# Kernel tuning notes

Hardware: AMD Instinct MI355X
Metric: run time of the kernel (lower is better)

## Reference

```python
import jax, jax.numpy as jnp
import numpy as np

NA, NT, E = 8000, 30000, 150000
H, C, HID = 4, 64, 64  # heads, per-head out_channels, hidden_dim
AF, TF = 32, 48


def _gat(x_src, x_dst, src, dst, W, a_src, a_dst, bias, n_dst):
    # PyG GATConv, concat=False, add_self_loops=False, eval (no dropout)
    h_src = (x_src @ W).reshape(-1, H, C)          # [Ns,H,C]
    h_dst = (x_dst @ W).reshape(-1, H, C)          # [Nd,H,C]
    al_s = jnp.sum(h_src * a_src, axis=-1)         # [Ns,H]
    al_d = jnp.sum(h_dst * a_dst, axis=-1)         # [Nd,H]
    e = jax.nn.leaky_relu(al_s[src] + al_d[dst], 0.2)  # [E,H]
    m = jax.ops.segment_max(e, dst, num_segments=n_dst)
    m = jnp.where(jnp.isfinite(m), m, 0.0)
    ex = jnp.exp(e - m[dst])
    den = jax.ops.segment_sum(ex, dst, num_segments=n_dst)
    alpha = ex / (den[dst] + 1e-16)                # per-dst softmax
    out = jax.ops.segment_sum(alpha[:, :, None] * h_src[src], dst, num_segments=n_dst)
    return jnp.mean(out, axis=1) + bias            # mean over heads + bias


def _bn(x, g, b):  # BatchNorm1d, training-mode batch stats, biased var
    mu = jnp.mean(x, axis=0)
    v = jnp.var(x, axis=0)
    return g * (x - mu) * jax.lax.rsqrt(v + 1e-5) + b


def _ln(x, g, b):
    mu = jnp.mean(x, axis=-1, keepdims=True)
    v = jnp.var(x, axis=-1, keepdims=True)
    return g * (x - mu) * jax.lax.rsqrt(v + 1e-5) + b


def setup_inputs() -> dict:
    key = jax.random.key(0)
    ks = jax.random.split(key, 40)
    n = lambda i, shp, s=0.05: jax.random.normal(ks[i], shp, jnp.float32) * s
    ri = lambda i, hi: jax.random.randint(ks[i], (E,), 0, hi, jnp.int32)
    inp = {
        'x_agent': jax.random.normal(ks[0], (NA, AF), jnp.float32),
        'x_track': jax.random.normal(ks[1], (NT, TF), jnp.float32),
        'ei_a2t1_src': ri(2, NA), 'ei_a2t1_dst': ri(3, NT),
        'ei_t2a1_src': ri(4, NT), 'ei_t2a1_dst': ri(5, NA),
        'ei_a2t2_src': ri(6, NA), 'ei_a2t2_dst': ri(7, NT),
        'ei_t2a2_src': ri(8, NT), 'ei_t2a2_dst': ri(9, NA),
        'ae_W': n(10, (AF, HID)), 'ae_b': jnp.zeros((HID,), jnp.float32),
        'te_W': n(11, (TF, HID)), 'te_b': jnp.zeros((HID,), jnp.float32),
        # stacked GATConv params: [layer=3, relation=4, ...]; rel order: a2t1,t2a1,a2t2,t2a2
        'conv_W': n(12, (3, 4, HID, H * C)),
        'conv_asrc': n(13, (3, 4, H, C)),
        'conv_adst': n(14, (3, 4, H, C)),
        'conv_bias': jnp.zeros((3, 4, C), jnp.float32),
        'bn_gamma': jnp.ones((3, 2, HID), jnp.float32),   # [layer, agent/track, HID]
        'bn_beta': jnp.zeros((3, 2, HID), jnp.float32),
        # actor heads: 0=agent_alpha,1=agent_beta,2=track_alpha,3=track_beta
        'actor_W1': n(15, (4, HID, HID // 2)), 'actor_b1': jnp.zeros((4, HID // 2), jnp.float32),
        'actor_g': jnp.ones((4, HID // 2), jnp.float32), 'actor_be': jnp.zeros((4, HID // 2), jnp.float32),
        'actor_W2': n(16, (4, HID // 2, 1)), 'actor_b2': jnp.zeros((4, 1), jnp.float32),
        # critic global value head
        'cW1': n(17, (HID * 6, HID * 2)), 'cb1': jnp.zeros((HID * 2,), jnp.float32),
        'cg1': jnp.ones((HID * 2,), jnp.float32), 'cbe1': jnp.zeros((HID * 2,), jnp.float32),
        'cW2': n(18, (HID * 2, HID)), 'cb2': jnp.zeros((HID,), jnp.float32),
        'cg2': jnp.ones((HID,), jnp.float32), 'cbe2': jnp.zeros((HID,), jnp.float32),
        'cW3': n(19, (HID, HID // 2)), 'cb3': jnp.zeros((HID // 2,), jnp.float32),
        'cW4': n(20, (HID // 2, 1)), 'cb4': jnp.zeros((1,), jnp.float32),
    }
    return inp


def _forward(x_agent, x_track,
             ei_a2t1_src, ei_a2t1_dst, ei_t2a1_src, ei_t2a1_dst,
             ei_a2t2_src, ei_a2t2_dst, ei_t2a2_src, ei_t2a2_dst,
             ae_W, ae_b, te_W, te_b,
             conv_W, conv_asrc, conv_adst, conv_bias,
             bn_gamma, bn_beta,
             actor_W1, actor_b1, actor_g, actor_be, actor_W2, actor_b2,
             cW1, cb1, cg1, cbe1, cW2, cb2, cg2, cbe2, cW3, cb3, cW4, cb4):
    xa = jax.nn.relu(x_agent @ ae_W + ae_b)
    xt = jax.nn.relu(x_track @ te_W + te_b)
    prev_a, prev_t = None, None
    for l in range(3):
        # HeteroConv aggr='mean': track <- mean(rel0, rel2); agent <- mean(rel1, rel3)
        ot = 0.5 * (_gat(xa, xt, ei_a2t1_src, ei_a2t1_dst, conv_W[l, 0], conv_asrc[l, 0], conv_adst[l, 0], conv_bias[l, 0], NT)
                    + _gat(xa, xt, ei_a2t2_src, ei_a2t2_dst, conv_W[l, 2], conv_asrc[l, 2], conv_adst[l, 2], conv_bias[l, 2], NT))
        oa = 0.5 * (_gat(xt, xa, ei_t2a1_src, ei_t2a1_dst, conv_W[l, 1], conv_asrc[l, 1], conv_adst[l, 1], conv_bias[l, 1], NA)
                    + _gat(xt, xa, ei_t2a2_src, ei_t2a2_dst, conv_W[l, 3], conv_asrc[l, 3], conv_adst[l, 3], conv_bias[l, 3], NA))
        oa = _bn(jax.nn.relu(oa), bn_gamma[l, 0], bn_beta[l, 0])
        ot = _bn(jax.nn.relu(ot), bn_gamma[l, 1], bn_beta[l, 1])
        if l > 0:  # residuals after layers 2 and 3
            oa = oa + prev_a
            ot = ot + prev_t
        prev_a, prev_t = oa, ot
        xa, xt = oa, ot

    def head(x, i):
        h = jax.nn.relu(_ln(x @ actor_W1[i] + actor_b1[i], actor_g[i], actor_be[i]))
        return jax.nn.softplus(h @ actor_W2[i] + actor_b2[i]) + 1.0

    aA, aB = head(xa, 0), head(xa, 1)
    tA, tB = head(xt, 2), head(xt, 3)
    aC = aA / (aA + aB)
    tC = tA / (tA + tB)

    # critic global value (torch.std is unbiased, ddof=1)
    g = jnp.concatenate([
        jnp.mean(xa, axis=0), jnp.max(xa, axis=0), jnp.std(xa, axis=0, ddof=1),
        jnp.mean(xt, axis=0), jnp.max(xt, axis=0), jnp.std(xt, axis=0, ddof=1)], axis=0)[None, :]
    h = jax.nn.relu(_ln(g @ cW1 + cb1, cg1, cbe1))
    h = jax.nn.relu(_ln(h @ cW2 + cb2, cg2, cbe2))
    h = jax.nn.relu(h @ cW3 + cb3)
    gv = jnp.squeeze(h @ cW4 + cb4)
    return aA, aB, aC, tA, tB, tC, gv


def reference(x_agent, x_track,
              ei_a2t1_src, ei_a2t1_dst, ei_t2a1_src, ei_t2a1_dst,
              ei_a2t2_src, ei_a2t2_dst, ei_t2a2_src, ei_t2a2_dst,
              ae_W, ae_b, te_W, te_b,
              conv_W, conv_asrc, conv_adst, conv_bias,
              bn_gamma, bn_beta,
              actor_W1, actor_b1, actor_g, actor_be, actor_W2, actor_b2,
              cW1, cb1, cg1, cbe1, cW2, cb2, cg2, cbe2, cW3, cb3, cW4, cb4):
    return _forward(x_agent, x_track,
                    ei_a2t1_src, ei_a2t1_dst, ei_t2a1_src, ei_t2a1_dst,
                    ei_a2t2_src, ei_a2t2_dst, ei_t2a2_src, ei_t2a2_dst,
                    ae_W, ae_b, te_W, te_b,
                    conv_W, conv_asrc, conv_adst, conv_bias,
                    bn_gamma, bn_beta,
                    actor_W1, actor_b1, actor_g, actor_be, actor_W2, actor_b2,
                    cW1, cb1, cg1, cbe1, cW2, cb2, cg2, cbe2, cW3, cb3, cW4, cb4)
```

## Files before the change

### kernel.cpp

```cpp
#include <hip/hip_runtime.h>
#include <math.h>

#define NAg 8000
#define NTr 30000
#define NE  150000

#define XA_OFF 0
#define XT_OFF 512000
#define H0_OFF 2432000
#define H1_OFF 4480000
#define H2_OFF 12160000
#define H3_OFF 14208000
#define BNSTB 8320000
#define WVB   8336384
#define ALS0 21888000
#define ALS1 21920000
#define ALS2 22040000
#define ALS3 22072000
#define ALD0 22192000
#define ALD1 22312000
#define ALD2 22344000
#define ALD3 22464000
#define ESRC_I 22496000
#define OAACC 23104000
#define OTACC 23616000
#define BNST 25536000
#define CST  25536256
#define ROWP_I 25536640
#define CURS_I 25656704
#define RELSTRIDE 30016

typedef unsigned short ushortT;

__device__ __forceinline__ float lrelu(float x){ return x >= 0.f ? x : 0.2f*x; }
__device__ __forceinline__ unsigned fmap(float f){ unsigned u=__float_as_uint(f); return (u&0x80000000u)? ~u : (u|0x80000000u); }
__device__ __forceinline__ float funmap(unsigned u){ return (u&0x80000000u)? __uint_as_float(u&0x7FFFFFFFu) : __uint_as_float(~u); }
__device__ __forceinline__ float softplusf(float x){ return fmaxf(x,0.f) + log1pf(expf(-fabsf(x))); }
__device__ __forceinline__ ushortT f2bf(float f){
  unsigned u = __float_as_uint(f);
  unsigned r = u + 0x7FFFu + ((u>>16)&1u);
  return (ushortT)(r>>16);
}
__device__ __forceinline__ float bf2f(ushortT s){ return __uint_as_float(((unsigned)s)<<16); }
__device__ __forceinline__ float wred64(float v){
  #pragma unroll
  for (int o=32;o;o>>=1) v += __shfl_xor(v,o);
  return v;
}
__device__ __forceinline__ float wred32(float v){
  #pragma unroll
  for (int o=16;o;o>>=1) v += __shfl_xor(v,o,32);
  return v;
}
__device__ __forceinline__ int selH(int r){ return r==0?H0_OFF: r==1?H1_OFF: r==2?H2_OFF:H3_OFF; }
__device__ __forceinline__ int selALS(int r){ return r==0?ALS0: r==1?ALS1: r==2?ALS2:ALS3; }
__device__ __forceinline__ int selALD(int r){ return r==0?ALD0: r==1?ALD1: r==2?ALD2:ALD3; }

__device__ __forceinline__ float agg_rel(const int* es, int p, int p1, const float* als,
                                         const ushortT* h16, float ad, int lane, int hh, int base) {
  float num0=0.f, num1=0.f, num2=0.f, num3=0.f, den=0.f;
  for (; p + 4 <= p1; p += 4) {
    int sa = es[p], sb = es[p+1], sc = es[p+2], sd4 = es[p+3];
    ushort4 va = *(const ushort4*)(h16 + (size_t)sa*256 + lane*4);
    ushort4 vb = *(const ushort4*)(h16 + (size_t)sb*256 + lane*4);
    ushort4 vc = *(const ushort4*)(h16 + (size_t)sc*256 + lane*4);
    ushort4 vd = *(const ushort4*)(h16 + (size_t)sd4*256 + lane*4);
    float la = als[sa*4+hh], lb = als[sb*4+hh], lc = als[sc*4+hh], ld = als[sd4*4+hh];
    float ea = __expf(lrelu(la + ad));
    float eb = __expf(lrelu(lb + ad));
    float ec = __expf(lrelu(lc + ad));
    float ed = __expf(lrelu(ld + ad));
    den += (ea+eb)+(ec+ed);
    float qa0=__shfl(ea,base), qa1=__shfl(ea,base+1), qa2=__shfl(ea,base+2), qa3=__shfl(ea,base+3);
    float qb0=__shfl(eb,base), qb1=__shfl(eb,base+1), qb2=__shfl(eb,base+2), qb3=__shfl(eb,base+3);
    float qc0=__shfl(ec,base), qc1=__shfl(ec,base+1), qc2=__shfl(ec,base+2), qc3=__shfl(ec,base+3);
    float qd0=__shfl(ed,base), qd1=__shfl(ed,base+1), qd2=__shfl(ed,base+2), qd3=__shfl(ed,base+3);
    num0 += qa0*bf2f(va.x) + qb0*bf2f(vb.x) + qc0*bf2f(vc.x) + qd0*bf2f(vd.x);
    num1 += qa1*bf2f(va.y) + qb1*bf2f(vb.y) + qc1*bf2f(vc.y) + qd1*bf2f(vd.y);
    num2 += qa2*bf2f(va.z) + qb2*bf2f(vb.z) + qc2*bf2f(vc.z) + qd2*bf2f(vd.z);
    num3 += qa3*bf2f(va.w) + qb3*bf2f(vb.w) + qc3*bf2f(vc.w) + qd3*bf2f(vd.w);
  }
  for (; p < p1; ++p) {
    int s = es[p];
    ushort4 va = *(const ushort4*)(h16 + (size_t)s*256 + lane*4);
    float e = __expf(lrelu(als[s*4 + hh] + ad));
    den += e;
    float q0 = __shfl(e, base), q1 = __shfl(e, base+1), q2 = __shfl(e, base+2), q3 = __shfl(e, base+3);
    num0 += q0*bf2f(va.x); num1 += q1*bf2f(va.y); num2 += q2*bf2f(va.z); num3 += q3*bf2f(va.w);
  }
  float rd = 1.f/(den + 1e-16f);
  float r0 = __shfl(rd, base), r1 = __shfl(rd, base+1), r2 = __shfl(rd, base+2), r3 = __shfl(rd, base+3);
  return num0*r0 + num1*r1 + num2*r2 + num3*r3;
}

__global__ __launch_bounds__(256) void k_encoder(const float* xA, const float* xT,
    const float* aeW, const float* aeB, const float* teW, const float* teB, float* ws) {
  int type = blockIdx.y;
  int N = type ? NTr : NAg;
  int t = threadIdx.x, wv = t >> 6, lane = t & 63;
  int n = blockIdx.x*4 + wv;
  int F = type ? 48 : 32;
  const float* X = type ? xT : xA;
  const float* W = type ? teW : aeW;
  const float* B = type ? teB : aeB;
  float* out = ws + (type ? XT_OFF : XA_OFF);
  __shared__ float xs[4][48];
  if (n < N && lane < F) xs[wv][lane] = X[(size_t)n*F + lane];
  __syncthreads();
  if (n >= N) return;
  float acc = B[lane];
  for (int k = 0; k < F; ++k) acc += xs[wv][k] * W[k*64 + lane];
  out[(size_t)n*64 + lane] = fmaxf(acc, 0.f);
}

__global__ __launch_bounds__(256) void k_hist(const int* d0_,const int* d1_,const int* d2_,const int* d3_,
                                              int* wsi) {
  int r = blockIdx.y;
  const int* dp = r==0? d0_ : r==1? d1_ : r==2? d2_ : d3_;
  int e = blockIdx.x*256 + threadIdx.x;
  if (e >= NE) return;
  atomicAdd(&wsi[ROWP_I + r*RELSTRIDE + dp[e]], 1);
}

__global__ __launch_bounds__(256) void k_scan(int* wsi) {
  int r = blockIdx.x;
  int n = ((r & 1) ? NAg : NTr) + 1;
  int* rp = wsi + ROWP_I + r*RELSTRIDE;
  __shared__ int part[256];
  int t = threadIdx.x;
  int chunk = (n + 255) / 256;
  int lo = t*chunk, hi = min(lo + chunk, n);
  int s = 0;
  for (int i = lo; i < hi; ++i) s += rp[i];
  part[t] = s;
  __syncthreads();
  if (t == 0) {
    int run = 0;
    for (int i = 0; i < 256; ++i) { int tm = part[i]; part[i] = run; run += tm; }
  }
  __syncthreads();
  int run = part[t];
  for (int i = lo; i < hi; ++i) { int tm = rp[i]; rp[i] = run; run += tm; }
}

__global__ __launch_bounds__(256) void k_fill(const int* s0,const int* d0_,const int* s1,const int* d1_,
    const int* s2,const int* d2_,const int* s3,const int* d3_, int* wsi) {
  int r = blockIdx.y;
  const int* sp = r==0? s0 : r==1? s1 : r==2? s2 : s3;
  const int* dp = r==0? d0_ : r==1? d1_ : r==2? d2_ : d3_;
  int e = blockIdx.x*256 + threadIdx.x;
  if (e >= NE) return;
  int d = dp[e];
  int pos = wsi[ROWP_I + r*RELSTRIDE + d] + atomicAdd(&wsi[CURS_I + r*RELSTRIDE + d], 1);
  wsi[ESRC_I + r*NE + pos] = sp[e];
}

__global__ __launch_bounds__(256) void k_wv(const float* convW, const float* convAsrc,
                                            const float* convAdst, float* ws) {
  int y = blockIdx.x, layer = blockIdx.y;
  int side = y >> 2, r = y & 3;
  const float* W  = convW + (size_t)(layer*4 + r)*64*256;
  const float* av = (side ? convAsrc : convAdst) + (size_t)(layer*4 + r)*256;
  int t = threadIdx.x;
  int k = t >> 2, h = t & 3;
  float s = 0.f;
  for (int c = 0; c < 64; ++c) s += W[k*256 + h*64 + c] * av[h*64 + c];
  ws[WVB + (size_t)(layer*8 + y)*256 + t] = s;
}

__global__ __launch_bounds__(256) void k_alx(float* ws, int layer) {
  int bid = blockIdx.x;
  int y, b0;
  if (bid < 7500)       { y = 0; b0 = bid; }
  else if (bid < 9500)  { y = 1; b0 = bid - 7500; }
  else if (bid < 17000) { y = 2; b0 = bid - 9500; }
  else if (bid < 19000) { y = 3; b0 = bid - 17000; }
  else if (bid < 21000) { y = 4; b0 = bid - 19000; }
  else if (bid < 28500) { y = 5; b0 = bid - 21000; }
  else if (bid < 30500) { y = 6; b0 = bid - 28500; }
  else                  { y = 7; b0 = bid - 30500; }
  int side = y >> 2, r = y & 3;
  int t = threadIdx.x, wv = t >> 6, lane = t & 63;
  int n = b0*4 + wv;
  const float* xv = ws + (side ? ((r & 1) ? XT_OFF : XA_OFF) : ((r & 1) ? XA_OFF : XT_OFF));
  float4 wv4 = *(const float4*)(ws + WVB + (size_t)(layer*8 + y)*256 + lane*4);
  float xk = xv[(size_t)n*64 + lane];
  float p0 = wred64(xk * wv4.x);
  float p1 = wred64(xk * wv4.y);
  float p2 = wred64(xk * wv4.z);
  float p3 = wred64(xk * wv4.w);
  if (lane == 0) {
    float4 o; o.x = p0; o.y = p1; o.z = p2; o.w = p3;
    *(float4*)(ws + (side ? selALS(r) : selALD(r)) + (size_t)n*4) = o;
  }
}

__global__ __launch_bounds__(256) void k_hgemm(const float* convW, float* ws, int layer) {
  int tile = blockIdx.x;
  int r, row0;
  if (tile < 500)        { r = 0; row0 = tile*16; }
  else if (tile < 2375)  { r = 1; row0 = (tile-500)*16; }
  else if (tile < 2875)  { r = 2; row0 = (tile-2375)*16; }
  else                   { r = 3; row0 = (tile-2875)*16; }
  const float* W  = convW + (size_t)(layer*4 + r)*64*256;
  const float* xg = ws + ((r & 1) ? XT_OFF : XA_OFF);
  ushortT* h16 = (ushortT*)(ws + selH(r));
  __shared__ float xs[16][64];
  int t = threadIdx.x;
  #pragma unroll
  for (int i = 0; i < 4; ++i) {
    int lin = i*256 + t;
    xs[lin>>6][lin&63] = xg[((size_t)row0 + (lin>>6))*64 + (lin&63)];
  }
  __syncthreads();
  int c0 = t & 63;
  int tr = t >> 6;
  float acc[4][4];
  #pragma unroll
  for (int i=0;i<4;i++){ acc[i][0]=0;acc[i][1]=0;acc[i][2]=0;acc[i][3]=0; }
  const float* Wc = W + c0;
  for (int k4 = 0; k4 < 16; ++k4) {
    float4 xv[4];
    #pragma unroll
    for (int i = 0; i < 4; ++i) xv[i] = *(const float4*)&xs[tr*4+i][k4*4];
    #pragma unroll
    for (int kk = 0; kk < 4; ++kk) {
      int k = k4*4 + kk;
      float w0 = Wc[k*256], w1 = Wc[k*256+64], w2 = Wc[k*256+128], w3 = Wc[k*256+192];
      #pragma unroll
      for (int i = 0; i < 4; ++i) {
        float x = (kk==0)?xv[i].x:(kk==1)?xv[i].y:(kk==2)?xv[i].z:xv[i].w;
        acc[i][0] += x*w0; acc[i][1] += x*w1; acc[i][2] += x*w2; acc[i][3] += x*w3;
      }
    }
  }
  #pragma unroll
  for (int i = 0; i < 4; ++i) {
    int row = row0 + tr*4 + i;
    ushort4 pk;
    pk.x = f2bf(acc[i][0]); pk.y = f2bf(acc[i][1]);
    pk.z = f2bf(acc[i][2]); pk.w = f2bf(acc[i][3]);
    *(ushort4*)(h16 + (size_t)row*256 + c0*4) = pk;
  }
}

__global__ __launch_bounds__(256) void k_agg(const float* convBias, float* ws, int layer) {
  int t = threadIdx.x, wv = t >> 6, lane = t & 63, hh = lane & 3, base = lane & ~3;
  const int* wsi = (const int*)ws;
  int bid = blockIdx.x;
  __shared__ float part[4][64];
  __shared__ float sh1[4][64];
  __shared__ float sh2[4][64];
  if (bid < 4000) {
    int node = bid*2 + (wv >> 1);
    int rr = wv & 1;
    int r = rr ? 3 : 1;
    const int* rp = wsi + ROWP_I + r*RELSTRIDE;
    const int* es = wsi + ESRC_I + r*NE;
    const float* als = ws + selALS(r);
    const ushortT* h16 = (const ushortT*)(ws + selH(r));
    float ad = (ws + selALD(r))[node*4 + hh];
    part[wv][lane] = agg_rel(es, rp[node], rp[node+1], als, h16, ad, lane, hh, base);
    __syncthreads();
    if (rr == 0) {
      float o = part[wv][lane] + part[wv+1][lane];
      float bavg = 0.5f*(convBias[(layer*4 + 1)*64 + lane] + convBias[(layer*4 + 3)*64 + lane]);
      float z = fmaxf(o*0.125f + bavg, 0.f);
      ws[OAACC + (size_t)node*64 + lane] = z;
      sh1[wv][lane] = z; sh2[wv][lane] = z*z;
    } else {
      sh1[wv][lane] = 0.f; sh2[wv][lane] = 0.f;
    }
    __syncthreads();
    if (t < 64) {
      float s1 = sh1[0][t] + sh1[1][t] + sh1[2][t] + sh1[3][t];
      float s2 = sh2[0][t] + sh2[1][t] + sh2[2][t] + sh2[3][t];
      int bucket = bid & 63;
      atomicAdd(&ws[BNSTB + bucket*256 + t], s1);
      atomicAdd(&ws[BNSTB + bucket*256 + 64 + t], s2);
    }
  } else {
    int node = (bid - 4000)*4 + wv;
    float outv = 0.f;
    #pragma unroll
    for (int rr = 0; rr < 2; ++rr) {
      int r = rr ? 2 : 0;
      const int* rp = wsi + ROWP_I + r*RELSTRIDE;
      const int* es = wsi + ESRC_I + r*NE;
      const float* als = ws + selALS(r);
      const ushortT* h16 = (const ushortT*)(ws + selH(r));
      float ad = (ws + selALD(r))[node*4 + hh];
      outv += agg_rel(es, rp[node], rp[node+1], als, h16, ad, lane, hh, base);
    }
    float bavg = 0.5f*(convBias[(layer*4 + 0)*64 + lane] + convBias[(layer*4 + 2)*64 + lane]);
    float z = fmaxf(outv*0.125f + bavg, 0.f);
    ws[OTACC + (size_t)node*64 + lane] = z;
    sh1[wv][lane] = z; sh2[wv][lane] = z*z;
    __syncthreads();
    if (t < 64) {
      float s1 = sh1[0][t] + sh1[1][t] + sh1[2][t] + sh1[3][t];
      float s2 = sh2[0][t] + sh2[1][t] + sh2[2][t] + sh2[3][t];
      int bucket = bid & 63;
      atomicAdd(&ws[BNSTB + bucket*256 + 128 + t], s1);
      atomicAdd(&ws[BNSTB + bucket*256 + 192 + t], s2);
    }
  }
}

__global__ __launch_bounds__(256) void k_bnred(float* ws) {
  int t = threadIdx.x;
  float s = 0.f;
  #pragma unroll
  for (int b = 0; b < 64; ++b) s += ws[BNSTB + b*256 + t];
  ws[BNST + t] = s;
}

__global__ __launch_bounds__(256) void k_bnnorm(const float* bnG, const float* bnB, float* ws, int layer) {
  int type = blockIdx.y;
  int N = type ? NTr : NAg;
  float* acc = ws + (type ? OTACC : OAACC);
  float* x = ws + (type ? XT_OFF : XA_OFF);
  int i = blockIdx.x*256 + threadIdx.x;
  if (i >= N*64) return;
  int c = i & 63;
  float Nf = (float)N;
  float s1 = ws[BNST + type*128 + c], s2 = ws[BNST + type*128 + 64 + c];
  float mu = s1/Nf, var = s2/Nf - mu*mu;
  float g = bnG[(layer*2 + type)*64 + c], b = bnB[(layer*2 + type)*64 + c];
  float y = g*(acc[i]-mu)*rsqrtf(var + 1e-5f) + b;
  if (layer > 0) y += x[i];
  x[i] = y;
}

__global__ __launch_bounds__(256) void k_actor(const float* aW1, const float* ab1, const float* ag,
    const float* abe, const float* aW2, const float* ab2, const float* ws, float* out) {
  int type = blockIdx.y;
  int N = type ? NTr : NAg;
  int t = threadIdx.x, wv = t >> 6, lane = t & 63;
  int p = lane >> 5, j = lane & 31;
  int n = blockIdx.x*4 + wv;
  const float* xg = ws + (type ? XT_OFF : XA_OFF);
  __shared__ float xsh[4][64];
  {
    int nn = blockIdx.x*4 + (t >> 6);
    if (nn < N) xsh[t >> 6][t & 63] = xg[(size_t)nn*64 + (t & 63)];
  }
  __syncthreads();
  if (n >= N) return;
  int i = (type ? 2 : 0) + p;
  const float* W = aW1 + i*2048 + j;
  float a0 = 0.f, a1 = 0.f, a2 = 0.f, a3 = 0.f;
  #pragma unroll
  for (int k = 0; k < 64; k += 4) {
    a0 += xsh[wv][k]   * W[k*32];
    a1 += xsh[wv][k+1] * W[(k+1)*32];
    a2 += xsh[wv][k+2] * W[(k+2)*32];
    a3 += xsh[wv][k+3] * W[(k+3)*32];
  }
  float tv = ((a0+a1)+(a2+a3)) + ab1[i*32 + j];
  float mu = wred32(tv) * (1.f/32.f);
  float dz = tv - mu;
  float var = wred32(dz*dz) * (1.f/32.f);
  float hn = fmaxf(ag[i*32+j]*dz*rsqrtf(var + 1e-5f) + abe[i*32+j], 0.f);
  float s = wred32(hn * aW2[i*32 + j]) + ab2[i];
  float val = softplusf(s) + 1.f;
  float vA = __shfl(val, 0);
  float vB = __shfl(val, 32);
  if (lane == 0) {
    int offA = type ? 24000 : 0, offB = type ? 54000 : 8000, offC = type ? 84000 : 16000;
    out[offA + n] = vA;
    out[offB + n] = vB;
    out[offC + n] = vA / (vA + vB);
  }
}

__global__ __launch_bounds__(256) void k_criticstats(float* ws) {
  int type = blockIdx.y;
  int N = type ? NTr : NAg;
  const float* x = ws + (type ? XT_OFF : XA_OFF);
  int t = threadIdx.x;
  int c = t & 63;
  float s1 = 0.f, s2 = 0.f, mx = -3.4e38f;
  for (int n = blockIdx.x*4 + (t>>6); n < N; n += gridDim.x*4) {
    float v = x[(size_t)n*64 + c];
    s1 += v; s2 += v*v; mx = fmaxf(mx, v);
  }
  __shared__ float sd[3][256];
  sd[0][t]=s1; sd[1][t]=s2; sd[2][t]=mx;
  __syncthreads();
  if (t < 64) {
    s1 = sd[0][t]+sd[0][t+64]+sd[0][t+128]+sd[0][t+192];
    s2 = sd[1][t]+sd[1][t+64]+sd[1][t+128]+sd[1][t+192];
    mx = fmaxf(fmaxf(sd[2][t],sd[2][t+64]), fmaxf(sd[2][t+128],sd[2][t+192]));
    atomicAdd(&ws[CST + type*192 + c], s1);
    atomicAdd(&ws[CST + type*192 + 64 + c], s2);
    atomicMax((unsigned*)&ws[CST + type*192 + 128 + c], fmap(mx));
  }
}

__device__ __forceinline__ float blocksum128(float v, float* red) {
  int t = threadIdx.x;
  red[t] = v; __syncthreads();
  #pragma unroll
  for (int s = 64; s > 0; s >>= 1) { if (t < s) red[t] += red[t+s]; __syncthreads(); }
  float r = red[0]; __syncthreads();
  return r;
}

__global__ __launch_bounds__(128) void k_critic(const float* cW1,const float* cb1,const float* cg1,const float* cbe1,
    const float* cW2,const float* cb2,const float* cg2,const float* cbe2,
    const float* cW3,const float* cb3,const float* cW4,const float* cb4,
    const float* ws, float* out) {
  __shared__ float g[384];
  __shared__ float h1[128];
  __shared__ float h2s[64];
  __shared__ float red[128];
  int t = threadIdx.x;
  if (t < 64) {
    #pragma unroll
    for (int type = 0; type < 2; ++type) {
      float Nf = type ? 30000.f : 8000.f;
      float s1 = ws[CST + type*192 + t];
      float s2 = ws[CST + type*192 + 64 + t];
      unsigned mu_ = __float_as_uint(ws[CST + type*192 + 128 + t]);
      float mean = s1 / Nf;
      float sd = sqrtf(fmaxf((s2 - Nf*mean*mean) / (Nf - 1.f), 0.f));
      g[type*192 + t] = mean;
      g[type*192 + 64 + t] = funmap(mu_);
      g[type*192 + 128 + t] = sd;
    }
  }
  __syncthreads();
  float v = cb1[t];
  for (int k = 0; k < 384; ++k) v += g[k] * cW1[k*128 + t];
  float mu = blocksum128(v, red) * (1.f/128.f);
  float d = v - mu;
  float var = blocksum128(d*d, red) * (1.f/128.f);
  h1[t] = fmaxf(cg1[t]*d*rsqrtf(var + 1e-5f) + cbe1[t], 0.f);
  __syncthreads();
  float v2 = 0.f;
  if (t < 64) { v2 = cb2[t]; for (int k = 0; k < 128; ++k) v2 += h1[k] * cW2[k*64 + t]; }
  float mu2 = blocksum128(t < 64 ? v2 : 0.f, red) * (1.f/64.f);
  float d2 = v2 - mu2;
  float var2 = blocksum128(t < 64 ? d2*d2 : 0.f, red) * (1.f/64.f);
  if (t < 64) h2s[t] = fmaxf(cg2[t]*d2*rsqrtf(var2 + 1e-5f) + cbe2[t], 0.f);
  __syncthreads();
  float v3 = 0.f;
  if (t < 32) {
    v3 = cb3[t];
    for (int k = 0; k < 64; ++k) v3 += h2s[k] * cW3[k*32 + t];
    v3 = fmaxf(v3, 0.f);
  }
  float s4 = blocksum128(t < 32 ? v3 * cW4[t] : 0.f, red);
  if (t == 0) out[114000] = s4 + cb4[0];
}

extern "C" void kernel_launch(void* const* d_in, const int* in_sizes, int n_in,
                              void* d_out, int out_size, void* d_ws, size_t ws_size,
                              hipStream_t stream) {
  const float* x_agent = (const float*)d_in[0];
  const float* x_track = (const float*)d_in[1];
  const int* s0 = (const int*)d_in[2]; const int* d0_ = (const int*)d_in[3];
  const int* s1 = (const int*)d_in[4]; const int* d1_ = (const int*)d_in[5];
  const int* s2 = (const int*)d_in[6]; const int* d2_ = (const int*)d_in[7];
  const int* s3 = (const int*)d_in[8]; const int* d3_ = (const int*)d_in[9];
  const float* aeW = (const float*)d_in[10]; const float* aeB = (const float*)d_in[11];
  const float* teW = (const float*)d_in[12]; const float* teB = (const float*)d_in[13];
  const float* convW    = (const float*)d_in[14];
  const float* convAsrc = (const float*)d_in[15];
  const float* convAdst = (const float*)d_in[16];
  const float* convBias = (const float*)d_in[17];
  const float* bnG = (const float*)d_in[18]; const float* bnB = (const float*)d_in[19];
  const float* aW1 = (const float*)d_in[20]; const float* ab1 = (const float*)d_in[21];
  const float* ag  = (const float*)d_in[22]; const float* abe = (const float*)d_in[23];
  const float* aW2 = (const float*)d_in[24]; const float* ab2 = (const float*)d_in[25];
  const float* cW1 = (const float*)d_in[26]; const float* cb1 = (const float*)d_in[27];
  const float* cg1 = (const float*)d_in[28]; const float* cbe1 = (const float*)d_in[29];
  const float* cW2 = (const float*)d_in[30]; const float* cb2 = (const float*)d_in[31];
  const float* cg2 = (const float*)d_in[32]; const float* cbe2 = (const float*)d_in[33];
  const float* cW3 = (const float*)d_in[34]; const float* cb3 = (const float*)d_in[35];
  const float* cW4 = (const float*)d_in[36]; const float* cb4 = (const float*)d_in[37];
  float* ws = (float*)d_ws;
  int* wsi = (int*)d_ws;
  float* out = (float*)d_out;

  hipMemsetAsync(wsi + ROWP_I, 0, (size_t)240128 * sizeof(int), stream);
  hipMemsetAsync(ws + CST, 0, (size_t)384 * sizeof(float), stream);

  k_encoder<<<dim3(7500, 2), 256, 0, stream>>>(x_agent, x_track, aeW, aeB, teW, teB, ws);

  k_hist<<<dim3(586, 4), 256, 0, stream>>>(d0_, d1_, d2_, d3_, wsi);
  k_scan<<<dim3(4), 256, 0, stream>>>(wsi);
  k_fill<<<dim3(586, 4), 256, 0, stream>>>(s0,d0_,s1,d1_,s2,d2_,s3,d3_, wsi);
  k_wv<<<dim3(8, 3), 256, 0, stream>>>(convW, convAsrc, convAdst, ws);

  for (int l = 0; l < 3; ++l) {
    hipMemsetAsync(ws + BNSTB, 0, (size_t)16384 * sizeof(float), stream);
    k_alx<<<dim3(38000), 256, 0, stream>>>(ws, l);
    k_hgemm<<<dim3(4750), 256, 0, stream>>>(convW, ws, l);
    k_agg<<<dim3(11500), 256, 0, stream>>>(convBias, ws, l);
    k_bnred<<<1, 256, 0, stream>>>(ws);
    k_bnnorm<<<dim3(7500, 2), 256, 0, stream>>>(bnG, bnB, ws, l);
  }

  k_criticstats<<<dim3(128, 2), 256, 0, stream>>>(ws);
  k_actor<<<dim3(7500, 2), 256, 0, stream>>>(aW1, ab1, ag, abe, aW2, ab2, ws, out);
  k_critic<<<1, 128, 0, stream>>>(cW1,cb1,cg1,cbe1,cW2,cb2,cg2,cbe2,cW3,cb3,cW4,cb4, ws, out);
}
```

Measured before the change: 668.7 us.

## Precompute per-edge exp weights and interleave conv weights for vector loads

```diff
diff --git a/kernel.cpp b/kernel.cpp
--- a/kernel.cpp
+++ b/kernel.cpp
@@ -13,6 +13,9 @@
 #define H3_OFF 14208000
 #define BNSTB 8320000
 #define WVB   8336384
+#define W2B   8342528
+#define EDST_I 13184000
+#define EXPS  18048000
 #define ALS0 21888000
 #define ALS1 21920000
 #define ALS2 22040000
@@ -56,40 +59,35 @@
 __device__ __forceinline__ int selALS(int r){ return r==0?ALS0: r==1?ALS1: r==2?ALS2:ALS3; }
 __device__ __forceinline__ int selALD(int r){ return r==0?ALD0: r==1?ALD1: r==2?ALD2:ALD3; }
 
-__device__ __forceinline__ float agg_rel(const int* es, int p, int p1, const float* als,
-                                         const ushortT* h16, float ad, int lane, int hh, int base) {
-  float num0=0.f, num1=0.f, num2=0.f, num3=0.f, den=0.f;
+__device__ __forceinline__ float agg_rel(const float4* ewp, int p, int p1,
+                                         const ushortT* h16, const int* es, int lane) {
+  float num0=0.f, num1=0.f, num2=0.f, num3=0.f;
+  float dn0=0.f, dn1=0.f, dn2=0.f, dn3=0.f;
   for (; p + 4 <= p1; p += 4) {
     int sa = es[p], sb = es[p+1], sc = es[p+2], sd4 = es[p+3];
+    float4 ea = ewp[p], eb = ewp[p+1], ec = ewp[p+2], ed = ewp[p+3];
     ushort4 va = *(const ushort4*)(h16 + (size_t)sa*256 + lane*4);
     ushort4 vb = *(const ushort4*)(h16 + (size_t)sb*256 + lane*4);
     ushort4 vc = *(const ushort4*)(h16 + (size_t)sc*256 + lane*4);
     ushort4 vd = *(const ushort4*)(h16 + (size_t)sd4*256 + lane*4);
-    float la = als[sa*4+hh], lb = als[sb*4+hh], lc = als[sc*4+hh], ld = als[sd4*4+hh];
-    float ea = __expf(lrelu(la + ad));
-    float eb = __expf(lrelu(lb + ad));
-    float ec = __expf(lrelu(lc + ad));
-    float ed = __expf(lrelu(ld + ad));
-    den += (ea+eb)+(ec+ed);
-    float qa0=__shfl(ea,base), qa1=__shfl(ea,base+1), qa2=__shfl(ea,base+2), qa3=__shfl(ea,base+3);
-    float qb0=__shfl(eb,base), qb1=__shfl(eb,base+1), qb2=__shfl(eb,base+2), qb3=__shfl(eb,base+3);
-    float qc0=__shfl(ec,base), qc1=__shfl(ec,base+1), qc2=__shfl(ec,base+2), qc3=__shfl(ec,base+3);
-    float qd0=__shfl(ed,base), qd1=__shfl(ed,base+1), qd2=__shfl(ed,base+2), qd3=__shfl(ed,base+3);
-    num0 += qa0*bf2f(va.x) + qb0*bf2f(vb.x) + qc0*bf2f(vc.x) + qd0*bf2f(vd.x);
-    num1 += qa1*bf2f(va.y) + qb1*bf2f(vb.y) + qc1*bf2f(vc.y) + qd1*bf2f(vd.y);
-    num2 += qa2*bf2f(va.z) + qb2*bf2f(vb.z) + qc2*bf2f(vc.z) + qd2*bf2f(vd.z);
-    num3 += qa3*bf2f(va.w) + qb3*bf2f(vb.w) + qc3*bf2f(vc.w) + qd3*bf2f(vd.w);
+    dn0 += (ea.x+eb.x)+(ec.x+ed.x);
+    dn1 += (ea.y+eb.y)+(ec.y+ed.y);
+    dn2 += (ea.z+eb.z)+(ec.z+ed.z);
+    dn3 += (ea.w+eb.w)+(ec.w+ed.w);
+    num0 += ea.x*bf2f(va.x) + eb.x*bf2f(vb.x) + ec.x*bf2f(vc.x) + ed.x*bf2f(vd.x);
+    num1 += ea.y*bf2f(va.y) + eb.y*bf2f(vb.y) + ec.y*bf2f(vc.y) + ed.y*bf2f(vd.y);
+    num2 += ea.z*bf2f(va.z) + eb.z*bf2f(vb.z) + ec.z*bf2f(vc.z) + ed.z*bf2f(vd.z);
+    num3 += ea.w*bf2f(va.w) + eb.w*bf2f(vb.w) + ec.w*bf2f(vc.w) + ed.w*bf2f(vd.w);
   }
   for (; p < p1; ++p) {
     int s = es[p];
+    float4 e4 = ewp[p];
     ushort4 va = *(const ushort4*)(h16 + (size_t)s*256 + lane*4);
-    float e = __expf(lrelu(als[s*4 + hh] + ad));
-    den += e;
-    float q0 = __shfl(e, base), q1 = __shfl(e, base+1), q2 = __shfl(e, base+2), q3 = __shfl(e, base+3);
-    num0 += q0*bf2f(va.x); num1 += q1*bf2f(va.y); num2 += q2*bf2f(va.z); num3 += q3*bf2f(va.w);
-  }
-  float rd = 1.f/(den + 1e-16f);
-  float r0 = __shfl(rd, base), r1 = __shfl(rd, base+1), r2 = __shfl(rd, base+2), r3 = __shfl(rd, base+3);
+    dn0 += e4.x; dn1 += e4.y; dn2 += e4.z; dn3 += e4.w;
+    num0 += e4.x*bf2f(va.x); num1 += e4.y*bf2f(va.y); num2 += e4.z*bf2f(va.z); num3 += e4.w*bf2f(va.w);
+  }
+  float r0 = 1.f/(dn0 + 1e-16f), r1 = 1.f/(dn1 + 1e-16f);
+  float r2 = 1.f/(dn2 + 1e-16f), r3 = 1.f/(dn3 + 1e-16f);
   return num0*r0 + num1*r1 + num2*r2 + num3*r3;
 }
 
@@ -153,6 +151,7 @@
   int d = dp[e];
   int pos = wsi[ROWP_I + r*RELSTRIDE + d] + atomicAdd(&wsi[CURS_I + r*RELSTRIDE + d], 1);
   wsi[ESRC_I + r*NE + pos] = sp[e];
+  wsi[EDST_I + r*NE + pos] = d;
 }
 
 __global__ __launch_bounds__(256) void k_wv(const float* convW, const float* convAsrc,
@@ -166,6 +165,15 @@
   float s = 0.f;
   for (int c = 0; c < 64; ++c) s += W[k*256 + h*64 + c] * av[h*64 + c];
   ws[WVB + (size_t)(layer*8 + y)*256 + t] = s;
+}
+
+__global__ __launch_bounds__(256) void k_wprep(const float* convW, float* ws) {
+  int lr = blockIdx.x;
+  const float* W = convW + (size_t)lr*64*256;
+  float* W2 = ws + W2B + (size_t)lr*64*256;
+  int t = threadIdx.x;
+  int c = t >> 2, h = t & 3;
+  for (int k = 0; k < 64; ++k) W2[k*256 + t] = W[k*256 + h*64 + c];
 }
 
 __global__ __launch_bounds__(256) void k_alx(float* ws, int layer) {
@@ -195,14 +203,31 @@
   }
 }
 
-__global__ __launch_bounds__(256) void k_hgemm(const float* convW, float* ws, int layer) {
+__global__ __launch_bounds__(256) void k_edgeexp(float* ws) {
+  int r = blockIdx.y;
+  int pos = blockIdx.x*256 + threadIdx.x;
+  if (pos >= NE) return;
+  const int* wsi = (const int*)ws;
+  int s = wsi[ESRC_I + r*NE + pos];
+  int d = wsi[EDST_I + r*NE + pos];
+  float4 a4 = *(const float4*)(ws + selALS(r) + (size_t)s*4);
+  float4 b4 = *(const float4*)(ws + selALD(r) + (size_t)d*4);
+  float4 o;
+  o.x = __expf(lrelu(a4.x + b4.x));
+  o.y = __expf(lrelu(a4.y + b4.y));
+  o.z = __expf(lrelu(a4.z + b4.z));
+  o.w = __expf(lrelu(a4.w + b4.w));
+  *(float4*)(ws + EXPS + ((size_t)r*NE + pos)*4) = o;
+}
+
+__global__ __launch_bounds__(256) void k_hgemm(float* ws, int layer) {
   int tile = blockIdx.x;
   int r, row0;
   if (tile < 500)        { r = 0; row0 = tile*16; }
   else if (tile < 2375)  { r = 1; row0 = (tile-500)*16; }
   else if (tile < 2875)  { r = 2; row0 = (tile-2375)*16; }
   else                   { r = 3; row0 = (tile-2875)*16; }
-  const float* W  = convW + (size_t)(layer*4 + r)*64*256;
+  const float* W2 = ws + W2B + (size_t)(layer*4 + r)*64*256;
   const float* xg = ws + ((r & 1) ? XT_OFF : XA_OFF);
   ushortT* h16 = (ushortT*)(ws + selH(r));
   __shared__ float xs[16][64];
@@ -218,7 +243,7 @@
   float acc[4][4];
   #pragma unroll
   for (int i=0;i<4;i++){ acc[i][0]=0;acc[i][1]=0;acc[i][2]=0;acc[i][3]=0; }
-  const float* Wc = W + c0;
+  const float* Wc = W2 + c0*4;
   for (int k4 = 0; k4 < 16; ++k4) {
     float4 xv[4];
     #pragma unroll
@@ -226,11 +251,11 @@
     #pragma unroll
     for (int kk = 0; kk < 4; ++kk) {
       int k = k4*4 + kk;
-      float w0 = Wc[k*256], w1 = Wc[k*256+64], w2 = Wc[k*256+128], w3 = Wc[k*256+192];
+      float4 w4 = *(const float4*)(Wc + k*256);
       #pragma unroll
       for (int i = 0; i < 4; ++i) {
         float x = (kk==0)?xv[i].x:(kk==1)?xv[i].y:(kk==2)?xv[i].z:xv[i].w;
-        acc[i][0] += x*w0; acc[i][1] += x*w1; acc[i][2] += x*w2; acc[i][3] += x*w3;
+        acc[i][0] += x*w4.x; acc[i][1] += x*w4.y; acc[i][2] += x*w4.z; acc[i][3] += x*w4.w;
       }
     }
   }
@@ -245,7 +270,7 @@
 }
 
 __global__ __launch_bounds__(256) void k_agg(const float* convBias, float* ws, int layer) {
-  int t = threadIdx.x, wv = t >> 6, lane = t & 63, hh = lane & 3, base = lane & ~3;
+  int t = threadIdx.x, wv = t >> 6, lane = t & 63;
   const int* wsi = (const int*)ws;
   int bid = blockIdx.x;
   __shared__ float part[4][64];
@@ -257,10 +282,9 @@
     int r = rr ? 3 : 1;
     const int* rp = wsi + ROWP_I + r*RELSTRIDE;
     const int* es = wsi + ESRC_I + r*NE;
-    const float* als = ws + selALS(r);
+    const float4* ewp = (const float4*)(ws + EXPS + (size_t)r*NE*4);
     const ushortT* h16 = (const ushortT*)(ws + selH(r));
-    float ad = (ws + selALD(r))[node*4 + hh];
-    part[wv][lane] = agg_rel(es, rp[node], rp[node+1], als, h16, ad, lane, hh, base);
+    part[wv][lane] = agg_rel(ewp, rp[node], rp[node+1], h16, es, lane);
     __syncthreads();
     if (rr == 0) {
       float o = part[wv][lane] + part[wv+1][lane];
@@ -287,10 +311,9 @@
       int r = rr ? 2 : 0;
       const int* rp = wsi + ROWP_I + r*RELSTRIDE;
       const int* es = wsi + ESRC_I + r*NE;
-      const float* als = ws + selALS(r);
+      const float4* ewp = (const float4*)(ws + EXPS + (size_t)r*NE*4);
       const ushortT* h16 = (const ushortT*)(ws + selH(r));
-      float ad = (ws + selALD(r))[node*4 + hh];
-      outv += agg_rel(es, rp[node], rp[node+1], als, h16, ad, lane, hh, base);
+      outv += agg_rel(ewp, rp[node], rp[node+1], h16, es, lane);
     }
     float bavg = 0.5f*(convBias[(layer*4 + 0)*64 + lane] + convBias[(layer*4 + 2)*64 + lane]);
     float z = fmaxf(outv*0.125f + bavg, 0.f);
@@ -493,11 +516,13 @@
   k_scan<<<dim3(4), 256, 0, stream>>>(wsi);
   k_fill<<<dim3(586, 4), 256, 0, stream>>>(s0,d0_,s1,d1_,s2,d2_,s3,d3_, wsi);
   k_wv<<<dim3(8, 3), 256, 0, stream>>>(convW, convAsrc, convAdst, ws);
+  k_wprep<<<dim3(12), 256, 0, stream>>>(convW, ws);
 
   for (int l = 0; l < 3; ++l) {
     hipMemsetAsync(ws + BNSTB, 0, (size_t)16384 * sizeof(float), stream);
     k_alx<<<dim3(38000), 256, 0, stream>>>(ws, l);
-    k_hgemm<<<dim3(4750), 256, 0, stream>>>(convW, ws, l);
+    k_edgeexp<<<dim3(586, 4), 256, 0, stream>>>(ws);
+    k_hgemm<<<dim3(4750), 256, 0, stream>>>(ws, l);
     k_agg<<<dim3(11500), 256, 0, stream>>>(convBias, ws, l);
     k_bnred<<<1, 256, 0, stream>>>(ws);
     k_bnnorm<<<dim3(7500, 2), 256, 0, stream>>>(bnG, bnB, ws, l);
```

After: 695.7 us. 1.04x slower.
